# Kernel tuning notes

Measured on AMD Instinct MI355X. Metric: run time of the kernel, lower is better.

The kernel has to match this reference:

```python
import jax, jax.numpy as jnp
import numpy as np

H = 8          # num_heads
EPS = 1e-6     # layernorm epsilon
NEG_INF = -1e9


def _ln(x, g, b):
    m = jnp.mean(x, axis=-1, keepdims=True)
    v = jnp.mean(jnp.square(x - m), axis=-1, keepdims=True)
    return g * (x - m) * jax.lax.rsqrt(v + EPS) + b


def _mha(xq, kv, wq, wk, wv, wo, bias):
    # xq: [B,Tq,D], kv: [B,Tk,D]; weights [D,D]. Returns (out [B,Tq,D], weights [B,H,Tq,Tk]).
    B, Tq, D = xq.shape
    dh = D // H
    q = (xq @ wq) * (dh ** -0.5)
    k = kv @ wk
    v = kv @ wv
    q = q.reshape(B, Tq, H, dh).transpose(0, 2, 1, 3)
    k = k.reshape(B, -1, H, dh).transpose(0, 2, 1, 3)
    v = v.reshape(B, -1, H, dh).transpose(0, 2, 1, 3)
    logits = jnp.einsum('bhqd,bhkd->bhqk', q, k)
    if bias is not None:
        logits = logits + bias
    w = jax.nn.softmax(logits, axis=-1)
    out = jnp.einsum('bhqk,bhkd->bhqd', w, v).transpose(0, 2, 1, 3).reshape(B, Tq, D)
    return out @ wo, w


def setup_inputs() -> dict:
    key = jax.random.key(0)
    ks = jax.random.split(key, 16)
    B, Td, Te, D, F, L = 2, 2048, 2048, 512, 2048, 2
    s = 0.02
    inp = {
        'x': jax.random.normal(ks[0], (B, Td, D), jnp.float32),
        'enc_a': jax.random.normal(ks[1], (B, Te, D), jnp.float32),
        'enc_c': jax.random.normal(ks[2], (B, Te, D), jnp.float32),
        'sa_wq': jax.random.normal(ks[3], (L, D, D), jnp.float32) * s,
        'sa_wk': jax.random.normal(ks[4], (L, D, D), jnp.float32) * s,
        'sa_wv': jax.random.normal(ks[5], (L, D, D), jnp.float32) * s,
        'sa_wo': jax.random.normal(ks[6], (L, D, D), jnp.float32) * s,
        'ed_wq': jax.random.normal(ks[7], (L, D, D), jnp.float32) * s,
        'ed_wk': jax.random.normal(ks[8], (L, D, D), jnp.float32) * s,
        'ed_wv': jax.random.normal(ks[9], (L, D, D), jnp.float32) * s,
        'ed_wo': jax.random.normal(ks[10], (L, D, D), jnp.float32) * s,
        'ffn_w1': jax.random.normal(ks[11], (L, D, F), jnp.float32) * s,
        'ffn_w2': jax.random.normal(ks[12], (L, F, D), jnp.float32) * s,
        'ln1_g': jnp.ones((L, D), jnp.float32), 'ln1_b': jnp.zeros((L, D), jnp.float32),
        'ln2_g': jnp.ones((L, D), jnp.float32), 'ln2_b': jnp.zeros((L, D), jnp.float32),
        'ln3_g': jnp.ones((L, D), jnp.float32), 'ln3_b': jnp.zeros((L, D), jnp.float32),
        'out_g': jnp.ones((D,), jnp.float32), 'out_b': jnp.zeros((D,), jnp.float32),
    }
    return inp


def reference(x, enc_a, enc_c, sa_wq, sa_wk, sa_wv, sa_wo, ed_wq, ed_wk, ed_wv, ed_wo,
              ffn_w1, ffn_w2, ln1_g, ln1_b, ln2_g, ln2_b, ln3_g, ln3_b, out_g, out_b):
    B, T, D = x.shape
    L = sa_wq.shape[0]
    # decoder self-attention causal bias, broadcast over [B,H]
    causal = jnp.where(jnp.tril(jnp.ones((T, T), bool)), 0.0, NEG_INF)[None, None]
    avg = None
    for i in range(L):
        h = _ln(x, ln1_g[i], ln1_b[i])
        y, _ = _mha(h, h, sa_wq[i], sa_wk[i], sa_wv[i], sa_wo[i], causal)
        x = x + y  # residual (dropout inactive at eval)
        h = _ln(x, ln2_g[i], ln2_b[i])
        y0, _ = _mha(h, enc_a, ed_wq[i], ed_wk[i], ed_wv[i], ed_wo[i], None)
        y1, w = _mha(h, enc_c, ed_wq[i], ed_wk[i], ed_wv[i], ed_wo[i], None)
        # original overwrites attn_scores with second call's head-averaged weights
        scores = jnp.mean(w, axis=1) / L
        avg = scores if avg is None else avg + scores
        x = x + y0 + y1
        h = _ln(x, ln3_g[i], ln3_b[i])
        x = x + jax.nn.relu(h @ ffn_w1[i]) @ ffn_w2[i]
    x = _ln(x, out_g, out_b)
    return x, avg
```

## Files before the change

kernel.cpp:

```cpp
#include <hip/hip_runtime.h>
#include <hip/hip_bf16.h>

#define BB 2
#define TT 2048
#define DD 512
#define FF 2048
#define HH 8
#define DH 64
#define LL 2
#define MM (BB*TT)

typedef __attribute__((ext_vector_type(8))) short bf16x8;
typedef __attribute__((ext_vector_type(4))) float f32x4;

__device__ __forceinline__ float bf2f(unsigned short u) {
    return __uint_as_float(((unsigned int)u) << 16);
}
__device__ __forceinline__ unsigned short f2bf(float f) {
    unsigned int u = __float_as_uint(f);
    u += 0x7fffu + ((u >> 16) & 1u);
    return (unsigned short)(u >> 16);
}
__device__ __forceinline__ unsigned int cvtpk(float a, float b) {
    unsigned int r;
    asm("v_cvt_pk_bf16_f32 %0, %1, %2" : "=v"(r) : "v"(a), "v"(b));
    return r;
}
__device__ __forceinline__ void gload16(const void* g, void* l) {
    __builtin_amdgcn_global_load_lds((__attribute__((address_space(1))) void*)g,
                                     (__attribute__((address_space(3))) void*)l, 16, 0, 0);
}

template<bool BF16OUT>
__global__ __launch_bounds__(256) void ln_kernel(const float* __restrict__ x,
                                                 const float* __restrict__ g,
                                                 const float* __restrict__ b,
                                                 void* __restrict__ out)
{
    const int row = blockIdx.x;
    const int tid = threadIdx.x;
    const float2 v = ((const float2*)(x + (size_t)row * DD))[tid];
    float s = v.x + v.y;
    float q = v.x * v.x + v.y * v.y;
    #pragma unroll
    for (int off = 32; off; off >>= 1) {
        s += __shfl_down(s, off);
        q += __shfl_down(q, off);
    }
    __shared__ float ss[4], qq[4];
    const int wid = tid >> 6;
    if ((tid & 63) == 0) { ss[wid] = s; qq[wid] = q; }
    __syncthreads();
    s = ss[0] + ss[1] + ss[2] + ss[3];
    q = qq[0] + qq[1] + qq[2] + qq[3];
    const float mean = s * (1.0f / DD);
    const float var = q * (1.0f / DD) - mean * mean;
    const float inv = rsqrtf(var + 1e-6f);
    const float2 gg = ((const float2*)g)[tid];
    const float2 bb = ((const float2*)b)[tid];
    const float ox = gg.x * (v.x - mean) * inv + bb.x;
    const float oy = gg.y * (v.y - mean) * inv + bb.y;
    if (BF16OUT) {
        const unsigned int pk = cvtpk(ox, oy);
        ((unsigned int*)((unsigned short*)out + (size_t)row * DD))[tid] = pk;
    } else {
        float2 o; o.x = ox; o.y = oy;
        ((float2*)((float*)out + (size_t)row * DD))[tid] = o;
    }
}

struct CvtEJob { const float* s; unsigned short* d; };
struct CvtEJobs2 { CvtEJob j[2]; };

__global__ __launch_bounds__(256) void cvt_kernel(CvtEJobs2 P, int n)
{
    const CvtEJob jb = P.j[blockIdx.z];
    const int i = (blockIdx.x * 256 + threadIdx.x) * 8;
    if (i >= n) return;
    const float4 a = *(const float4*)(jb.s + i);
    const float4 b = *(const float4*)(jb.s + i + 4);
    unsigned int o[4];
    o[0] = cvtpk(a.x, a.y); o[1] = cvtpk(a.z, a.w);
    o[2] = cvtpk(b.x, b.y); o[3] = cvtpk(b.z, b.w);
    *(bf16x8*)(jb.d + i) = *(bf16x8*)o;
}

struct CvtTJob { const float* s; unsigned short* d; int K; int N; };
struct CvtTJobs20 { CvtTJob j[20]; };

__global__ __launch_bounds__(256) void cvtT_kernel(CvtTJobs20 P)
{
    __shared__ float t[32][33];
    const CvtTJob jb = P.j[blockIdx.z];
    const int gk = blockIdx.y << 5, gn = blockIdx.x << 5;
    if (gk >= jb.K || gn >= jb.N) return;
    const int tx = threadIdx.x & 31, ty = threadIdx.x >> 5;
    #pragma unroll
    for (int i = 0; i < 4; ++i)
        t[ty + i * 8][tx] = jb.s[(size_t)(gk + ty + i * 8) * jb.N + gn + tx];
    __syncthreads();
    #pragma unroll
    for (int i = 0; i < 4; ++i)
        jb.d[(size_t)(gn + ty + i * 8) * jb.K + gk + tx] = f2bf(t[tx][ty + i * 8]);
}

struct GemmJob {
    const unsigned short* A;
    const unsigned short* Wt;
    const float* res;
    float* Cf;
    unsigned short* Cb;
    unsigned short* Ct;
    float scale;
    int relu;
};
struct GemmJobs8 { GemmJob j[8]; };

__global__ __launch_bounds__(256, 2) void gemm_mfma(GemmJobs8 P, int M, int N, int K)
{
    __shared__ __align__(16) unsigned char lds[32768];
    const GemmJob jb = P.j[blockIdx.z];
    const int tid = threadIdx.x, lane = tid & 63, w = tid >> 6;
    const int bn = blockIdx.x << 7, bm = blockIdx.y << 7;
    const int wr = (w >> 1) << 6, wc = (w & 1) << 6;
    const size_t strA = (size_t)K * 2;

    f32x4 acc[4][4] = {};
    const int akey = (lane & 7) << 4;
    const int frow = lane & 15;
    const int kq = (lane >> 4) << 4;

    for (int kt = 0; kt < K; kt += 64) {
        __syncthreads();
        #pragma unroll
        for (int c = 0; c < 4; ++c) {
            const int q = c * 4 + w;
            const int o = (q << 10) + (lane << 4);
            const int row = o >> 7;
            const int colb = (o & 127) ^ ((row & 7) << 4);
            gload16((const char*)jb.A + (size_t)(bm + row) * strA + kt * 2 + colb,
                    lds + (q << 10));
            gload16((const char*)jb.Wt + (size_t)(bn + row) * strA + kt * 2 + colb,
                    lds + 16384 + (q << 10));
        }
        asm volatile("s_waitcnt vmcnt(0)" ::: "memory");
        __syncthreads();
        #pragma unroll
        for (int kk = 0; kk < 2; ++kk) {
            bf16x8 av[4], bv[4];
            #pragma unroll
            for (int i = 0; i < 4; ++i) {
                const int rA = wr + (i << 4) + frow;
                av[i] = *(const bf16x8*)(lds + (rA << 7) + ((((kk << 6) + kq)) ^ akey));
                const int rB = wc + (i << 4) + frow;
                bv[i] = *(const bf16x8*)(lds + 16384 + (rB << 7) + ((((kk << 6) + kq)) ^ akey));
            }
            #pragma unroll
            for (int i = 0; i < 4; ++i)
                #pragma unroll
                for (int j = 0; j < 4; ++j)
                    acc[i][j] = __builtin_amdgcn_mfma_f32_16x16x32_bf16(av[i], bv[j], acc[i][j], 0, 0, 0);
        }
    }

    const int crow0 = (lane >> 4) << 2;
    const int ccol = lane & 15;
    if (jb.Ct) {
        #pragma unroll
        for (int i = 0; i < 4; ++i)
            #pragma unroll
            for (int j = 0; j < 4; ++j) {
                const int gm = bm + wr + (i << 4) + crow0;
                const int gn = bn + wc + (j << 4) + ccol;
                const int bI = gm >> 11, t = gm & 2047;
                const int hI = gn >> 6, d = gn & 63;
                uint2 pk;
                pk.x = cvtpk(acc[i][j][0], acc[i][j][1]);
                pk.y = cvtpk(acc[i][j][2], acc[i][j][3]);
                *(uint2*)(jb.Ct + ((size_t)((bI * HH + hI) * DH + d)) * TT + t) = pk;
            }
        return;
    }
    #pragma unroll
    for (int i = 0; i < 4; ++i) {
        #pragma unroll
        for (int j = 0; j < 4; ++j) {
            #pragma unroll
            for (int r = 0; r < 4; ++r) {
                const int gm = bm + wr + (i << 4) + crow0 + r;
                const int gn = bn + wc + (j << 4) + ccol;
                float v = acc[i][j][r] * jb.scale;
                if (jb.relu) v = fmaxf(v, 0.f);
                const size_t idx = (size_t)gm * N + gn;
                if (jb.res) v += jb.res[idx];
                if (jb.Cf) jb.Cf[idx] = v;
                if (jb.Cb) jb.Cb[idx] = f2bf(v);
            }
        }
    }
}

template<bool CAUSAL, bool DUAL, int NQ>
__global__ __launch_bounds__(256, (NQ == 1) ? 4 : 3) void flash_mfma(
    const unsigned short* __restrict__ q,
    const unsigned short* __restrict__ ka, const unsigned short* __restrict__ vta,
    const unsigned short* __restrict__ kc, const unsigned short* __restrict__ vtc,
    unsigned short* __restrict__ Opart,
    float* __restrict__ mlpart)
{
    __shared__ __align__(16) char lds[(NQ == 1) ? 40960 : 49152];
    const int tid = threadIdx.x;
    const int lane = tid & 63, w = tid >> 6;
    const int g4 = lane >> 4, c = lane & 15;

    constexpr int GX = (32 / NQ) * 2;
    const int f = blockIdx.x + GX * (blockIdx.y + 8 * blockIdx.z);
    const int xcd = f & 7;
    const int tt = f >> 3;
    const int u = tt % GX;
    const int half = u & 1, jq = u >> 1;
    const int grp = (tt / GX) * 8 + xcd;
    int b, h, which;
    if (DUAL) { which = grp & 1; b = (grp >> 1) & 1; h = grp >> 2; }
    else      { which = 0;       b = grp & 1;        h = grp >> 1; }
    const int q0 = jq * (64 * NQ);
    const int q0w = q0 + w * (16 * NQ);
    const int kendw = q0w + 16 * NQ;

    const unsigned short* k  = (DUAL && which) ? kc : ka;
    const unsigned short* vt = (DUAL && which) ? vtc : vta;
    const int slot = (DUAL ? (which << 1) : 0) + half;
    unsigned short* Od = Opart + (size_t)slot * MM * DD;
    float* mld = mlpart + (size_t)slot * (BB * HH * TT * 2);

    bf16x8 Qf[NQ][2];
    #pragma unroll
    for (int jb = 0; jb < NQ; ++jb) {
        const unsigned short* qp = q + (size_t)(b * TT + q0w + (jb << 4) + c) * DD + h * DH + (g4 << 3);
        Qf[jb][0] = *(const bf16x8*)qp;
        Qf[jb][1] = *(const bf16x8*)(qp + 32);
    }
    const char* kbase = (const char*)(k + (size_t)b * TT * DD + h * DH);
    const char* vtb   = (const char*)(vt + (size_t)(b * HH + h) * DH * TT);
    char* Pw = lds + 32768 + w * (NQ * 2048);
    const int pkey = (c & 7) << 4;

    f32x4 O[NQ][4] = {};
    float mval[NQ], lpart[NQ];
    #pragma unroll
    for (int jb = 0; jb < NQ; ++jb) { mval[jb] = -1e30f; lpart[jb] = 0.f; }

    const int ntt = CAUSAL ? ((q0 + 64 * NQ) >> 6) : (TT >> 6);
    const int tBeg = half ? ((ntt + 1) >> 1) : 0;
    const int tEnd = half ? ntt : ((ntt + 1) >> 1);

    auto STAGE = [&](int t, int sel) {
        const int kt = t << 6;
        char* Kb = lds + sel * 8192;
        char* Vb = lds + 16384 + sel * 8192;
        #pragma unroll
        for (int c8 = 0; c8 < 2; ++c8) {
            const int qc = (c8 << 2) + w;
            const int o = (qc << 10) + (lane << 4);
            const int row = o >> 7;
            const int colb = (o & 127) ^ ((row & 7) << 4);
            gload16(kbase + (size_t)(kt + row) * (DD * 2) + colb, Kb + (qc << 10));
            gload16(vtb + (size_t)row * (TT * 2) + kt * 2 + colb, Vb + (qc << 10));
        }
    };

    if (tBeg < tEnd) {
        STAGE(tBeg, 0);
        asm volatile("s_waitcnt vmcnt(0)" ::: "memory");
        __syncthreads();

        for (int t = tBeg; t < tEnd; ++t) {
            const int cur = (t - tBeg) & 1;
            if (t + 1 < tEnd) STAGE(t + 1, cur ^ 1);
            const int kt = t << 6;

            if (!CAUSAL || kt < kendw) {
                const char* Kb = lds + cur * 8192;
                const char* Vb = lds + 16384 + cur * 8192;

                f32x4 s[NQ][4] = {};
                #pragma unroll
                for (int kk = 0; kk < 2; ++kk) {
                    bf16x8 av[4];
                    #pragma unroll
                    for (int i = 0; i < 4; ++i) {
                        const int r = (i << 4) + c;
                        av[i] = *(const bf16x8*)(Kb + (r << 7) + (((kk << 6) + (g4 << 4)) ^ ((r & 7) << 4)));
                    }
                    #pragma unroll
                    for (int i = 0; i < 4; ++i)
                        #pragma unroll
                        for (int jb = 0; jb < NQ; ++jb)
                            s[jb][i] = __builtin_amdgcn_mfma_f32_16x16x32_bf16(av[i], Qf[jb][kk], s[jb][i], 0, 0, 0);
                }

                #pragma unroll
                for (int jb = 0; jb < NQ; ++jb) {
                    const int qbase = q0w + (jb << 4);
                    if (CAUSAL && kt + 63 > qbase) {
                        #pragma unroll
                        for (int i = 0; i < 4; ++i)
                            #pragma unroll
                            for (int r = 0; r < 4; ++r)
                                if (kt + (i << 4) + (g4 << 2) + r > qbase + c) s[jb][i][r] = -1e30f;
                    }
                    float pmax = -1e30f;
                    #pragma unroll
                    for (int i = 0; i < 4; ++i)
                        #pragma unroll
                        for (int r = 0; r < 4; ++r) pmax = fmaxf(pmax, s[jb][i][r]);
                    if (__any(pmax > mval[jb] + 11.f)) {
                        float mx = fmaxf(pmax, __shfl_xor(pmax, 16));
                        mx = fmaxf(mx, __shfl_xor(mx, 32));
                        const float mn = fmaxf(mval[jb], mx);
                        const float scf = exp2f(mval[jb] - mn);
                        lpart[jb] *= scf;
                        #pragma unroll
                        for (int r = 0; r < 4; ++r) {
                            const float fr = __shfl(scf, (g4 << 2) + r);
                            #pragma unroll
                            for (int jj = 0; jj < 4; ++jj) O[jb][jj][r] *= fr;
                        }
                        mval[jb] = mn;
                    }
                    float ps = 0.f;
                    #pragma unroll
                    for (int i = 0; i < 4; ++i)
                        #pragma unroll
                        for (int r = 0; r < 4; ++r) {
                            const float p = exp2f(s[jb][i][r] - mval[jb]);
                            s[jb][i][r] = p;
                            ps += p;
                        }
                    lpart[jb] += ps;
                    #pragma unroll
                    for (int i = 0; i < 4; ++i) {
                        uint2 pk;
                        pk.x = cvtpk(s[jb][i][0], s[jb][i][1]);
                        pk.y = cvtpk(s[jb][i][2], s[jb][i][3]);
                        const int baddr = (((jb << 4) + c) << 7) + (((i << 4) + (g4 << 2)) << 1);
                        *(uint2*)(Pw + (baddr ^ pkey)) = pk;
                    }
                }
                asm volatile("s_waitcnt lgkmcnt(0)" ::: "memory");
                __builtin_amdgcn_sched_barrier(0);

                #pragma unroll
                for (int kk = 0; kk < 2; ++kk) {
                    bf16x8 pa[NQ];
                    #pragma unroll
                    for (int jb = 0; jb < NQ; ++jb)
                        pa[jb] = *(const bf16x8*)(Pw + (((((jb << 4) + c) << 7) + (kk << 6) + (g4 << 4)) ^ pkey));
                    #pragma unroll
                    for (int jj = 0; jj < 4; ++jj) {
                        const int d = (jj << 4) + c;
                        const bf16x8 vb = *(const bf16x8*)(Vb + (d << 7) + (((kk << 6) + (g4 << 4)) ^ ((d & 7) << 4)));
                        #pragma unroll
                        for (int jb = 0; jb < NQ; ++jb)
                            O[jb][jj] = __builtin_amdgcn_mfma_f32_16x16x32_bf16(pa[jb], vb, O[jb][jj], 0, 0, 0);
                    }
                }
            }

            asm volatile("s_waitcnt vmcnt(0)" ::: "memory");
            __syncthreads();
        }
    }

    #pragma unroll
    for (int jb = 0; jb < NQ; ++jb) {
        float l2 = lpart[jb] + __shfl_xor(lpart[jb], 16);
        const float ltot = l2 + __shfl_xor(l2, 32);
        #pragma unroll
        for (int jj = 0; jj < 4; ++jj)
            #pragma unroll
            for (int r = 0; r < 4; ++r) {
                const int qr = q0w + (jb << 4) + (g4 << 2) + r;
                Od[(size_t)(b * TT + qr) * DD + h * DH + (jj << 4) + c] = f2bf(O[jb][jj][r]);
            }
        if (lane < 16) {
            const size_t mi = (((size_t)b * HH + h) * TT + q0w + (jb << 4) + lane) * 2;
            mld[mi] = mval[jb];
            mld[mi + 1] = ltot;
        }
    }
}

template<int NS>
__global__ __launch_bounds__(256) void merge_kernel(
    const unsigned short* __restrict__ Opart, const float* __restrict__ mlpart,
    unsigned short* __restrict__ out)
{
    const int row = blockIdx.x;
    const int b = row >> 11, rt = row & 2047;
    const int t = threadIdx.x;
    const int d0 = t << 1, h = d0 >> 6;
    float acc0 = 0.f, acc1 = 0.f;
    #pragma unroll
    for (int s = 0; s < NS; ++s) {
        const size_t mb = ((size_t)(b * HH + h) * TT + rt) * 2;
        const float* mp0 = mlpart + (size_t)(s * 2 + 0) * (BB * HH * TT * 2) + mb;
        const float* mp1 = mlpart + (size_t)(s * 2 + 1) * (BB * HH * TT * 2) + mb;
        const float m0 = mp0[0], l0 = mp0[1], m1 = mp1[0], l1 = mp1[1];
        const float M = fmaxf(m0, m1);
        const float a0 = exp2f(m0 - M), a1 = exp2f(m1 - M);
        const float inv = 1.f / (a0 * l0 + a1 * l1);
        const unsigned short* p0 = Opart + (size_t)(s * 2 + 0) * MM * DD + (size_t)row * DD + d0;
        const unsigned short* p1 = Opart + (size_t)(s * 2 + 1) * MM * DD + (size_t)row * DD + d0;
        acc0 += (a0 * bf2f(p0[0]) + a1 * bf2f(p1[0])) * inv;
        acc1 += (a0 * bf2f(p0[1]) + a1 * bf2f(p1[1])) * inv;
    }
    ((unsigned int*)(out + (size_t)row * DD))[t] = cvtpk(acc0, acc1);
}

__global__ __launch_bounds__(64) void avg_mfma_kernel(const unsigned short* __restrict__ qm,
                                                      const unsigned short* __restrict__ kcm,
                                                      const float* __restrict__ mlpart,
                                                      float* __restrict__ avg, int first)
{
    __shared__ __align__(16) unsigned char ldsQ[2][8192];
    __shared__ __align__(16) unsigned char ldsK[2][8192];
    __shared__ float sM[8][64];
    __shared__ float sIL[8][64];
    const int lane = threadIdx.x;

    const int f = blockIdx.x + 32 * (blockIdx.y + 32 * blockIdx.z);
    const int xcd = f & 7, t = f >> 3;
    const int b = xcd >> 2;
    const int q0 = (((xcd & 3) << 3) + (t >> 5)) << 6;
    const int kt0 = (t & 31) << 6;

    #pragma unroll
    for (int h = 0; h < 8; ++h) {
        const size_t mb = ((size_t)(b * HH + h) * TT + q0 + lane) * 2;
        const float* mp2 = mlpart + (size_t)2 * (BB * HH * TT * 2) + mb;
        const float* mp3 = mlpart + (size_t)3 * (BB * HH * TT * 2) + mb;
        const float m2 = mp2[0], l2v = mp2[1], m3 = mp3[0], l3v = mp3[1];
        const float M = fmaxf(m2, m3);
        const float L = exp2f(m2 - M) * l2v + exp2f(m3 - M) * l3v;
        sM[h][lane] = M;
        sIL[h][lane] = 1.f / L;
    }

    float avac[4][4][4] = {};
    const int akey = (lane & 7) << 4;
    const int frow = lane & 15;
    const int kq = (lane >> 4) << 4;
    const int crow0 = (lane >> 4) << 2;

    auto STAGE = [&](int h, int sel) {
        #pragma unroll
        for (int c = 0; c < 8; ++c) {
            const int o = (c << 10) + (lane << 4);
            const int row = o >> 7;
            const int colb = (o & 127) ^ ((row & 7) << 4);
            gload16((const char*)qm + ((size_t)(b * TT + q0 + row) * DD + h * DH) * 2 + colb,
                    &ldsQ[sel][c << 10]);
            gload16((const char*)kcm + ((size_t)(b * TT + kt0 + row) * DD + h * DH) * 2 + colb,
                    &ldsK[sel][c << 10]);
        }
    };

    asm volatile("s_waitcnt vmcnt(0)" ::: "memory");
    STAGE(0, 0);

    for (int h = 0; h < 8; ++h) {
        const int cur = h & 1;
        if (h < 7) {
            STAGE(h + 1, cur ^ 1);
            asm volatile("s_waitcnt vmcnt(16)" ::: "memory");
        } else {
            asm volatile("s_waitcnt vmcnt(0)" ::: "memory");
        }
        __builtin_amdgcn_sched_barrier(0);

        f32x4 s[4][4] = {};
        #pragma unroll
        for (int kk = 0; kk < 2; ++kk) {
            bf16x8 qv[4], kv[4];
            #pragma unroll
            for (int i = 0; i < 4; ++i) {
                qv[i] = *(const bf16x8*)(&ldsQ[cur][(((i << 4) + frow) << 7) + (((kk << 6) + kq) ^ akey)]);
                kv[i] = *(const bf16x8*)(&ldsK[cur][(((i << 4) + frow) << 7) + (((kk << 6) + kq) ^ akey)]);
            }
            #pragma unroll
            for (int i = 0; i < 4; ++i)
                #pragma unroll
                for (int j = 0; j < 4; ++j)
                    s[i][j] = __builtin_amdgcn_mfma_f32_16x16x32_bf16(qv[i], kv[j], s[i][j], 0, 0, 0);
        }
        #pragma unroll
        for (int i = 0; i < 4; ++i)
            #pragma unroll
            for (int j = 0; j < 4; ++j)
                #pragma unroll
                for (int r = 0; r < 4; ++r) {
                    const int qr = (i << 4) + crow0 + r;
                    avac[i][j][r] += exp2f(s[i][j][r] - sM[h][qr]) * sIL[h][qr];
                }
        __builtin_amdgcn_sched_barrier(0);
    }

    float* dst = avg + ((size_t)b * TT + q0) * TT + kt0;
    #pragma unroll
    for (int i = 0; i < 4; ++i)
        #pragma unroll
        for (int j = 0; j < 4; ++j)
            #pragma unroll
            for (int r = 0; r < 4; ++r) {
                const int qr = (i << 4) + crow0 + r;
                const int kc = (j << 4) + (lane & 15);
                const float v = avac[i][j][r] * (1.f / (HH * LL));
                float* p = dst + (size_t)qr * TT + kc;
                *p = first ? v : (*p + v);
            }
}

extern "C" void kernel_launch(void* const* d_in, const int* in_sizes, int n_in,
                              void* d_out, int out_size, void* d_ws, size_t ws_size,
                              hipStream_t stream)
{
    const float* x_in   = (const float*)d_in[0];
    const float* enc_a  = (const float*)d_in[1];
    const float* enc_c  = (const float*)d_in[2];
    const float* sa_wq0 = (const float*)d_in[3];
    const float* sa_wk0 = (const float*)d_in[4];
    const float* sa_wv0 = (const float*)d_in[5];
    const float* sa_wo0 = (const float*)d_in[6];
    const float* ed_wq0 = (const float*)d_in[7];
    const float* ed_wk0 = (const float*)d_in[8];
    const float* ed_wv0 = (const float*)d_in[9];
    const float* ed_wo0 = (const float*)d_in[10];
    const float* ffn_w10 = (const float*)d_in[11];
    const float* ffn_w20 = (const float*)d_in[12];
    const float* ln1_g0 = (const float*)d_in[13];
    const float* ln1_b0 = (const float*)d_in[14];
    const float* ln2_g0 = (const float*)d_in[15];
    const float* ln2_b0 = (const float*)d_in[16];
    const float* ln3_g0 = (const float*)d_in[17];
    const float* ln3_b0 = (const float*)d_in[18];
    const float* out_g  = (const float*)d_in[19];
    const float* out_b  = (const float*)d_in[20];

    const size_t NTD = (size_t)MM * DD;
    const size_t MB = 1u << 20;
    char* W = (char*)d_ws;
    float*          x_buf   = (float*)(W);
    unsigned short* h_bf    = (unsigned short*)(W + 8 * MB);
    unsigned short* q_bf    = (unsigned short*)(W + 12 * MB);
    unsigned short* k1_bf   = (unsigned short*)(W + 16 * MB);
    unsigned short* vt1     = (unsigned short*)(W + 20 * MB);
    unsigned short* k2_bf   = (unsigned short*)(W + 24 * MB);
    unsigned short* vt2     = (unsigned short*)(W + 28 * MB);
    unsigned short* attnA   = (unsigned short*)(W + 32 * MB);
    unsigned short* attnS   = (unsigned short*)(W + 36 * MB);
    unsigned short* encA_bf = (unsigned short*)(W + 41 * MB);
    unsigned short* encC_bf = (unsigned short*)(W + 45 * MB);
    unsigned short* wbf     = (unsigned short*)(W + 49 * MB);
    unsigned short* Opart   = (unsigned short*)(W + 68 * MB);
    float*          mlpart  = (float*)(W + 84 * MB);
    unsigned short* ffn_bf  = q_bf;

    const bool fused = (ws_size >= (size_t)97 * MB);
    unsigned short* k1c  = fused ? (unsigned short*)(W + 88 * MB) : k1_bf;
    unsigned short* vt1c = fused ? (unsigned short*)(W + 92 * MB) : vt1;

    unsigned short* w1t = wbf + (size_t)16 * DD * DD;
    unsigned short* w2t = w1t + (size_t)2 * DD * FF;
    auto wd = [&](int l, int which) { return wbf + ((size_t)(l * 8 + which)) * DD * DD; };

    float* x_out   = (float*)d_out;
    float* avg_out = (float*)d_out + NTD;

    hipMemcpyAsync(x_buf, x_in, NTD * sizeof(float), hipMemcpyDeviceToDevice, stream);

    {
        CvtTJobs20 J{};
        const float* srcs[8] = {sa_wq0, sa_wk0, sa_wv0, sa_wo0, ed_wq0, ed_wk0, ed_wv0, ed_wo0};
        for (int l = 0; l < LL; ++l)
            for (int t = 0; t < 8; ++t)
                J.j[l * 8 + t] = {srcs[t] + (size_t)l * DD * DD, wd(l, t), DD, DD};
        for (int l = 0; l < LL; ++l) {
            J.j[16 + l] = {ffn_w10 + (size_t)l * DD * FF, w1t + (size_t)l * FF * DD, DD, FF};
            J.j[18 + l] = {ffn_w20 + (size_t)l * FF * DD, w2t + (size_t)l * DD * FF, FF, DD};
        }
        cvtT_kernel<<<dim3(FF / 32, FF / 32, 20), 256, 0, stream>>>(J);
    }
    {
        CvtEJobs2 J{};
        J.j[0] = {enc_a, encA_bf};
        J.j[1] = {enc_c, encC_bf};
        cvt_kernel<<<dim3(NTD / 8 / 256, 1, 2), 256, 0, stream>>>(J, (int)NTD);
    }

    const dim3 flashSelfG(64, HH, BB);
    const dim3 flashCrossG(32, HH, BB * 2);
    const dim3 avgG(TT / 64, TT / 64, BB);
    const float qscale = 0.125f * 1.4426950408889634f;

    for (int i = 0; i < LL; ++i) {
        const size_t fOff = (size_t)i * DD * FF;
        const size_t lOff = (size_t)i * DD;

        ln_kernel<true><<<MM, 256, 0, stream>>>(x_buf, ln1_g0 + lOff, ln1_b0 + lOff, h_bf);
        if (fused) {
            GemmJobs8 J{};
            J.j[0] = {h_bf,    wd(i, 0), nullptr, nullptr, q_bf, nullptr, qscale, 0};
            J.j[1] = {h_bf,    wd(i, 1), nullptr, nullptr, k1_bf, nullptr, 1.f, 0};
            J.j[2] = {h_bf,    wd(i, 2), nullptr, nullptr, nullptr, vt1, 1.f, 0};
            J.j[3] = {encA_bf, wd(i, 5), nullptr, nullptr, k1c, nullptr, 1.f, 0};
            J.j[4] = {encA_bf, wd(i, 6), nullptr, nullptr, nullptr, vt1c, 1.f, 0};
            J.j[5] = {encC_bf, wd(i, 5), nullptr, nullptr, k2_bf, nullptr, 1.f, 0};
            J.j[6] = {encC_bf, wd(i, 6), nullptr, nullptr, nullptr, vt2, 1.f, 0};
            gemm_mfma<<<dim3(DD / 128, MM / 128, 7), 256, 0, stream>>>(J, MM, DD, DD);
        } else {
            GemmJobs8 J{};
            J.j[0] = {h_bf, wd(i, 0), nullptr, nullptr, q_bf, nullptr, qscale, 0};
            J.j[1] = {h_bf, wd(i, 1), nullptr, nullptr, k1_bf, nullptr, 1.f, 0};
            J.j[2] = {h_bf, wd(i, 2), nullptr, nullptr, nullptr, vt1, 1.f, 0};
            gemm_mfma<<<dim3(DD / 128, MM / 128, 3), 256, 0, stream>>>(J, MM, DD, DD);
        }
        flash_mfma<true, false, 1><<<flashSelfG, 256, 0, stream>>>(
            q_bf, k1_bf, vt1, nullptr, nullptr, Opart, mlpart);
        merge_kernel<1><<<MM, 256, 0, stream>>>(Opart, mlpart, attnA);
        {
            GemmJobs8 J{};
            J.j[0] = {attnA, wd(i, 3), x_buf, x_buf, nullptr, nullptr, 1.f, 0};
            gemm_mfma<<<dim3(DD / 128, MM / 128, 1), 256, 0, stream>>>(J, MM, DD, DD);
        }

        ln_kernel<true><<<MM, 256, 0, stream>>>(x_buf, ln2_g0 + lOff, ln2_b0 + lOff, h_bf);
        if (fused) {
            GemmJobs8 J{};
            J.j[0] = {h_bf, wd(i, 4), nullptr, nullptr, q_bf, nullptr, qscale, 0};
            gemm_mfma<<<dim3(DD / 128, MM / 128, 1), 256, 0, stream>>>(J, MM, DD, DD);
        } else {
            GemmJobs8 J{};
            J.j[0] = {h_bf,    wd(i, 4), nullptr, nullptr, q_bf, nullptr, qscale, 0};
            J.j[1] = {encA_bf, wd(i, 5), nullptr, nullptr, k1_bf, nullptr, 1.f, 0};
            J.j[2] = {encA_bf, wd(i, 6), nullptr, nullptr, nullptr, vt1, 1.f, 0};
            J.j[3] = {encC_bf, wd(i, 5), nullptr, nullptr, k2_bf, nullptr, 1.f, 0};
            J.j[4] = {encC_bf, wd(i, 6), nullptr, nullptr, nullptr, vt2, 1.f, 0};
            gemm_mfma<<<dim3(DD / 128, MM / 128, 5), 256, 0, stream>>>(J, MM, DD, DD);
        }
        flash_mfma<false, true, 2><<<flashCrossG, 256, 0, stream>>>(
            q_bf, k1c, vt1c, k2_bf, vt2, Opart, mlpart);
        merge_kernel<2><<<MM, 256, 0, stream>>>(Opart, mlpart, attnS);
        avg_mfma_kernel<<<avgG, 64, 0, stream>>>(q_bf, k2_bf, mlpart, avg_out, (i == 0) ? 1 : 0);
        {
            GemmJobs8 J{};
            J.j[0] = {attnS, wd(i, 7), x_buf, x_buf, nullptr, nullptr, 1.f, 0};
            gemm_mfma<<<dim3(DD / 128, MM / 128, 1), 256, 0, stream>>>(J, MM, DD, DD);
        }

        ln_kernel<true><<<MM, 256, 0, stream>>>(x_buf, ln3_g0 + lOff, ln3_b0 + lOff, h_bf);
        {
            GemmJobs8 J{};
            J.j[0] = {h_bf, w1t + fOff, nullptr, nullptr, ffn_bf, nullptr, 1.f, 1};
            gemm_mfma<<<dim3(FF / 128, MM / 128, 1), 256, 0, stream>>>(J, MM, FF, DD);
        }
        {
            GemmJobs8 J{};
            J.j[0] = {ffn_bf, w2t + fOff, x_buf, x_buf, nullptr, nullptr, 1.f, 0};
            gemm_mfma<<<dim3(DD / 128, MM / 128, 1), 256, 0, stream>>>(J, MM, DD, FF);
        }
    }

    ln_kernel<false><<<MM, 256, 0, stream>>>(x_buf, out_g, out_b, x_out);
}
```

Measured before the change: 688.1 us.

## Share Q tile across four waves in head-averaged attention weight kernel

The head-averaged attention-weight kernel moves from 64-thread blocks over a 32x32x2 grid to 256-thread blocks over 512 blocks, where four waves share one staged Q tile in LDS and each handles its own key tile. This cuts redundant Q loads and the per-block m/l softmax-stats recomputation by a factor of four. In exchange it drops the double-buffered prefetch in favour of synchronous staging with two block barriers per head, which exposes global load latency.

```diff
diff --git a/kernel.cpp b/kernel.cpp
--- a/kernel.cpp
+++ b/kernel.cpp
@@ -418,33 +418,36 @@
     ((unsigned int*)(out + (size_t)row * DD))[t] = cvtpk(acc0, acc1);
 }
 
-__global__ __launch_bounds__(64) void avg_mfma_kernel(const unsigned short* __restrict__ qm,
-                                                      const unsigned short* __restrict__ kcm,
-                                                      const float* __restrict__ mlpart,
-                                                      float* __restrict__ avg, int first)
-{
-    __shared__ __align__(16) unsigned char ldsQ[2][8192];
-    __shared__ __align__(16) unsigned char ldsK[2][8192];
+__global__ __launch_bounds__(256) void avg_mfma_kernel(const unsigned short* __restrict__ qm,
+                                                       const unsigned short* __restrict__ kcm,
+                                                       const float* __restrict__ mlpart,
+                                                       float* __restrict__ avg, int first)
+{
+    __shared__ __align__(16) unsigned char ldsQ[8192];
+    __shared__ __align__(16) unsigned char ldsK[4][8192];
     __shared__ float sM[8][64];
     __shared__ float sIL[8][64];
-    const int lane = threadIdx.x;
-
-    const int f = blockIdx.x + 32 * (blockIdx.y + 32 * blockIdx.z);
+    const int tid = threadIdx.x;
+    const int lane = tid & 63, w = tid >> 6;
+
+    const int f = blockIdx.x;
     const int xcd = f & 7, t = f >> 3;
     const int b = xcd >> 2;
-    const int q0 = (((xcd & 3) << 3) + (t >> 5)) << 6;
-    const int kt0 = (t & 31) << 6;
-
-    #pragma unroll
-    for (int h = 0; h < 8; ++h) {
-        const size_t mb = ((size_t)(b * HH + h) * TT + q0 + lane) * 2;
+    const int q0 = ((((xcd & 3) << 3) + (t >> 3))) << 6;
+    const int kt0 = (((t & 7) << 2) + w) << 6;
+
+    #pragma unroll
+    for (int u = 0; u < 2; ++u) {
+        const int e = (u << 8) + tid;
+        const int h = e >> 6, r = e & 63;
+        const size_t mb = ((size_t)(b * HH + h) * TT + q0 + r) * 2;
         const float* mp2 = mlpart + (size_t)2 * (BB * HH * TT * 2) + mb;
         const float* mp3 = mlpart + (size_t)3 * (BB * HH * TT * 2) + mb;
         const float m2 = mp2[0], l2v = mp2[1], m3 = mp3[0], l3v = mp3[1];
         const float M = fmaxf(m2, m3);
         const float L = exp2f(m2 - M) * l2v + exp2f(m3 - M) * l3v;
-        sM[h][lane] = M;
-        sIL[h][lane] = 1.f / L;
+        sM[h][r] = M;
+        sIL[h][r] = 1.f / L;
     }
 
     float avac[4][4][4] = {};
@@ -453,31 +456,27 @@
     const int kq = (lane >> 4) << 4;
     const int crow0 = (lane >> 4) << 2;
 
-    auto STAGE = [&](int h, int sel) {
-        #pragma unroll
-        for (int c = 0; c < 8; ++c) {
-            const int o = (c << 10) + (lane << 4);
+    for (int h = 0; h < 8; ++h) {
+        __syncthreads();
+        #pragma unroll
+        for (int u = 0; u < 2; ++u) {
+            const int ch = (u << 2) + w;
+            const int o = (ch << 10) + (lane << 4);
             const int row = o >> 7;
             const int colb = (o & 127) ^ ((row & 7) << 4);
             gload16((const char*)qm + ((size_t)(b * TT + q0 + row) * DD + h * DH) * 2 + colb,
-                    &ldsQ[sel][c << 10]);
+                    ldsQ + (ch << 10));
+        }
+        #pragma unroll
+        for (int c8 = 0; c8 < 8; ++c8) {
+            const int o = (c8 << 10) + (lane << 4);
+            const int row = o >> 7;
+            const int colb = (o & 127) ^ ((row & 7) << 4);
             gload16((const char*)kcm + ((size_t)(b * TT + kt0 + row) * DD + h * DH) * 2 + colb,
-                    &ldsK[sel][c << 10]);
-        }
-    };
-
-    asm volatile("s_waitcnt vmcnt(0)" ::: "memory");
-    STAGE(0, 0);
-
-    for (int h = 0; h < 8; ++h) {
-        const int cur = h & 1;
-        if (h < 7) {
-            STAGE(h + 1, cur ^ 1);
-            asm volatile("s_waitcnt vmcnt(16)" ::: "memory");
-        } else {
-            asm volatile("s_waitcnt vmcnt(0)" ::: "memory");
-        }
-        __builtin_amdgcn_sched_barrier(0);
+                    &ldsK[w][c8 << 10]);
+        }
+        asm volatile("s_waitcnt vmcnt(0)" ::: "memory");
+        __syncthreads();
 
         f32x4 s[4][4] = {};
         #pragma unroll
@@ -485,8 +484,8 @@
             bf16x8 qv[4], kv[4];
             #pragma unroll
             for (int i = 0; i < 4; ++i) {
-                qv[i] = *(const bf16x8*)(&ldsQ[cur][(((i << 4) + frow) << 7) + (((kk << 6) + kq) ^ akey)]);
-                kv[i] = *(const bf16x8*)(&ldsK[cur][(((i << 4) + frow) << 7) + (((kk << 6) + kq) ^ akey)]);
+                qv[i] = *(const bf16x8*)(ldsQ + (((i << 4) + frow) << 7) + (((kk << 6) + kq) ^ akey));
+                kv[i] = *(const bf16x8*)(&ldsK[w][(((i << 4) + frow) << 7) + (((kk << 6) + kq) ^ akey)]);
             }
             #pragma unroll
             for (int i = 0; i < 4; ++i)
@@ -503,7 +502,6 @@
                     const int qr = (i << 4) + crow0 + r;
                     avac[i][j][r] += exp2f(s[i][j][r] - sM[h][qr]) * sIL[h][qr];
                 }
-        __builtin_amdgcn_sched_barrier(0);
     }
 
     float* dst = avg + ((size_t)b * TT + q0) * TT + kt0;
@@ -600,7 +598,6 @@
 
     const dim3 flashSelfG(64, HH, BB);
     const dim3 flashCrossG(32, HH, BB * 2);
-    const dim3 avgG(TT / 64, TT / 64, BB);
     const float qscale = 0.125f * 1.4426950408889634f;
 
     for (int i = 0; i < LL; ++i) {
@@ -651,7 +648,7 @@
         flash_mfma<false, true, 2><<<flashCrossG, 256, 0, stream>>>(
             q_bf, k1c, vt1c, k2_bf, vt2, Opart, mlpart);
         merge_kernel<2><<<MM, 256, 0, stream>>>(Opart, mlpart, attnS);
-        avg_mfma_kernel<<<avgG, 64, 0, stream>>>(q_bf, k2_bf, mlpart, avg_out, (i == 0) ? 1 : 0);
+        avg_mfma_kernel<<<512, 256, 0, stream>>>(q_bf, k2_bf, mlpart, avg_out, (i == 0) ? 1 : 0);
         {
             GemmJobs8 J{};
             J.j[0] = {attnS, wd(i, 7), x_buf, x_buf, nullptr, nullptr, 1.f, 0};
```

New measurement: 688.1 us. Within noise of the previous version (-0.0%).
